# Optimization experiments

Measured on AMD Instinct MI355X. Metric: run time of the kernel, lower is better.

## Reference

```python
import jax, jax.numpy as jnp
import numpy as np

B, S, D_MODEL = 4, 1024, 1024
N_HEAD, D_HEAD = 16, 64
ALL_HEAD = N_HEAD * D_HEAD
SCALE = 1.0 / (D_HEAD ** 0.5)
LN_EPS = 1e-5


def setup_inputs() -> dict:
    key = jax.random.key(0)
    ks = jax.random.split(key, 8)
    inp = jax.random.normal(ks[0], (B, S, D_MODEL), dtype=jnp.float32)
    attn_mask = jax.random.randint(ks[1], (B, S), 0, 2, dtype=jnp.int32)
    w = lambda k, shp: (jax.random.normal(k, shp, dtype=jnp.float32) * 0.02)
    Wq = w(ks[2], (D_MODEL, ALL_HEAD)); bq = jnp.zeros((ALL_HEAD,), jnp.float32)
    Wk = w(ks[3], (D_MODEL, ALL_HEAD)); bk = jnp.zeros((ALL_HEAD,), jnp.float32)
    Wv = w(ks[4], (D_MODEL, ALL_HEAD)); bv = jnp.zeros((ALL_HEAD,), jnp.float32)
    Wo = w(ks[5], (ALL_HEAD, D_MODEL))
    ln_g = jnp.ones((D_MODEL,), jnp.float32)
    ln_b = jnp.zeros((D_MODEL,), jnp.float32)
    return {"inp": inp, "attn_mask": attn_mask, "Wq": Wq, "bq": bq,
            "Wk": Wk, "bk": bk, "Wv": Wv, "bv": bv, "Wo": Wo,
            "ln_g": ln_g, "ln_b": ln_b}


def _layer_norm(x, g, b):
    mu = jnp.mean(x, axis=-1, keepdims=True)
    var = jnp.mean((x - mu) ** 2, axis=-1, keepdims=True)
    return (x - mu) * jax.lax.rsqrt(var + LN_EPS) * g + b


def reference(inp, attn_mask, Wq, bq, Wk, bk, Wv, bv, Wo, ln_g, ln_b):
    residual = inp
    # QKV projections -> [B, S, H, D] -> flat [B*H, S, D] (batch-major, as torch permute+reshape)
    def proj(W, bias):
        h = (inp @ W + bias).reshape(B, S, N_HEAD, D_HEAD)
        return h.transpose(0, 2, 1, 3).reshape(B * N_HEAD, S, D_HEAD)
    q = proj(Wq, bq)
    k = proj(Wk, bk)
    v = proj(Wv, bv)
    # scores [B*H, S, S]
    scores = jnp.einsum('bqd,bkd->bqk', q, k) * SCALE
    # key-padding mask: nonzero -> masked_fill(-100000.0)
    mask = (attn_mask.astype(scores.dtype) != 0)  # [B, S]
    mask = jnp.broadcast_to(mask[:, None, None, :], (B, N_HEAD, S, S))
    mask = mask.reshape(B * N_HEAD, S, S)
    scores = jnp.where(mask, jnp.float32(-100000.0), scores)
    probs = jax.nn.softmax(scores, axis=2)  # dropout is identity in eval
    attn_vec = jnp.einsum('bqk,bkd->bqd', probs, v)  # [B*H, S, D]
    # faithful to torch: view(n_head, B, S, d_head).permute(1,2,0,3)
    attn_vec = attn_vec.reshape(N_HEAD, B, S, D_HEAD).transpose(1, 2, 0, 3)
    attn_vec = attn_vec.reshape(B, S, ALL_HEAD)
    attn_out = attn_vec @ Wo  # o_net has no bias; output dropout identity
    # post-lnorm (pre_lnorm=False)
    return _layer_norm(residual + attn_out, ln_g, ln_b)
```

## Files before the change

### kernel.cpp

```cpp
#include <hip/hip_runtime.h>

typedef __attribute__((ext_vector_type(8))) short bf16x8;
typedef __attribute__((ext_vector_type(4))) float f32x4;
typedef __attribute__((ext_vector_type(16))) float f32x16;

#define D_MODEL 1024
#define SEQ 1024
#define NB 4
#define NH 16
#define DH 64
#define MROWS 4096

__device__ __forceinline__ unsigned short f2bf(float f) {
    union { float f; unsigned u; } x; x.f = f;
    unsigned r = x.u + 0x7fffu + ((x.u >> 16) & 1u);
    return (unsigned short)(r >> 16);
}

__device__ __forceinline__ void gload16(const void* g, void* l) {
    __builtin_amdgcn_global_load_lds((const __attribute__((address_space(1))) void*)g,
                                     (__attribute__((address_space(3))) void*)l, 16, 0, 0);
}

__device__ __forceinline__ float xhalf(float x, int hi) {
    float a = x, b = x;
    asm volatile("v_permlane32_swap_b32 %0, %1" : "+v"(a), "+v"(b));
    return hi ? b : a;
}

__global__ __launch_bounds__(256) void cvt_x(const float* __restrict__ x,
                                             unsigned short* __restrict__ o) {
    int i = blockIdx.x * 256 + threadIdx.x;
    float4 v = ((const float4*)x)[i];
    ushort4 r;
    r.x = f2bf(v.x); r.y = f2bf(v.y); r.z = f2bf(v.z); r.w = f2bf(v.w);
    ((ushort4*)o)[i] = r;
}

__global__ __launch_bounds__(256) void pack_mask(const int* __restrict__ amask,
                                                 unsigned long long* __restrict__ mwords) {
    int word = blockIdx.x * 4 + (threadIdx.x >> 6);
    int lane = threadIdx.x & 63;
    unsigned long long m = __ballot(amask[word * 64 + lane] != 0);
    if (lane == 0) mwords[word] = m;
}

__global__ __launch_bounds__(256) void transpose_w(const float* __restrict__ Wq,
                                                   const float* __restrict__ Wk,
                                                   const float* __restrict__ Wv,
                                                   const float* __restrict__ Wo,
                                                   unsigned short* __restrict__ Wqkv_t,
                                                   unsigned short* __restrict__ Wo_t) {
    __shared__ float tile[32][33];
    const int mtx = blockIdx.z;
    const float* src = mtx == 0 ? Wq : mtx == 1 ? Wk : mtx == 2 ? Wv : Wo;
    unsigned short* dst = mtx < 3 ? (Wqkv_t + (size_t)mtx * D_MODEL * D_MODEL) : Wo_t;
    const int n0 = blockIdx.x * 32, k0 = blockIdx.y * 32;
    const int tx = threadIdx.x, ty = threadIdx.y;
    #pragma unroll
    for (int i = 0; i < 32; i += 8)
        tile[ty + i][tx] = src[(size_t)(k0 + ty + i) * D_MODEL + n0 + tx];
    __syncthreads();
    #pragma unroll
    for (int i = 0; i < 32; i += 8)
        dst[(size_t)(n0 + ty + i) * D_MODEL + k0 + tx] = f2bf(tile[tx][ty + i]);
}

#define CSW(r, c) ((r) * 128 + ((c) ^ (((r) & 7) << 3)))

__global__ __launch_bounds__(256) void gemm_qkv(const unsigned short* __restrict__ Xb,
                                                const unsigned short* __restrict__ Wt,
                                                const float* __restrict__ bq,
                                                const float* __restrict__ bk,
                                                const float* __restrict__ bv,
                                                unsigned short* __restrict__ Qb,
                                                unsigned short* __restrict__ Kb,
                                                unsigned short* __restrict__ Vt) {
    __shared__ unsigned short SM[32768];
    const int tid = threadIdx.x;
    const int lane = tid & 63, wid = tid >> 6;
    const int fr = lane & 15, fg = lane >> 4;
    const int wr = wid >> 1, wc = wid & 1;
    const int lin = blockIdx.x;
    const int x = lin & 7, i = lin >> 3;
    const int bxm = (x & 3) * 8 + (i & 7);
    const int byn = (x >> 2) * 12 + (i >> 3);
    const int m0 = bxm * 128, n0 = byn * 128;
    const unsigned short* Ag = Xb + (size_t)m0 * D_MODEL;
    const unsigned short* Bg = Wt + (size_t)n0 * D_MODEL;
    const int srow = tid >> 3;
    const int scol = 8 * ((tid & 7) ^ ((tid >> 3) & 7));
    f32x4 acc[4][4] = {};

#define QSTAGE(bf, kt2)                                                                   \
    {                                                                                     \
        const int kb = (kt2) * 64;                                                        \
        _Pragma("unroll")                                                                 \
        for (int j = 0; j < 4; ++j) {                                                     \
            int row = j * 32 + srow;                                                      \
            gload16(Ag + (size_t)row * D_MODEL + kb + scol, &SM[(bf) * 16384 + (j * 256 + tid) * 8]); \
            gload16(Bg + (size_t)row * D_MODEL + kb + scol, &SM[(bf) * 16384 + 8192 + (j * 256 + tid) * 8]); \
        }                                                                                 \
    }

    QSTAGE(0, 0);
    __syncthreads();
    int buf = 0;
    for (int kt = 0; kt < 16; ++kt) {
        if (kt < 15) QSTAGE(buf ^ 1, kt + 1);
        const unsigned short* As = &SM[buf * 16384];
        const unsigned short* Bs = &SM[buf * 16384 + 8192];
        #pragma unroll
        for (int ks = 0; ks < 2; ++ks) {
            bf16x8 af[4], bfv[4];
            #pragma unroll
            for (int m = 0; m < 4; ++m) {
                int row = wr * 64 + m * 16 + fr;
                af[m] = *(const bf16x8*)&As[row * 64 + ((ks * 32 + fg * 8) ^ ((row & 7) * 8))];
            }
            #pragma unroll
            for (int n = 0; n < 4; ++n) {
                int row = wc * 64 + n * 16 + fr;
                bfv[n] = *(const bf16x8*)&Bs[row * 64 + ((ks * 32 + fg * 8) ^ ((row & 7) * 8))];
            }
            __builtin_amdgcn_s_setprio(1);
            #pragma unroll
            for (int m = 0; m < 4; ++m)
                #pragma unroll
                for (int n = 0; n < 4; ++n)
                    acc[m][n] = __builtin_amdgcn_mfma_f32_16x16x32_bf16(af[m], bfv[n], acc[m][n], 0, 0, 0);
            __builtin_amdgcn_s_setprio(0);
        }
        __syncthreads();
        buf ^= 1;
    }
#undef QSTAGE
    unsigned short* Cs = SM;
    const int sel = n0 >> 10;
    const int npb = n0 & 1023;
    if (sel < 2) {
        #pragma unroll
        for (int n = 0; n < 4; ++n) {
            int cn = wc * 64 + n * 16 + fr;
            float bias = (sel == 0 ? bq : bk)[npb + cn];
            #pragma unroll
            for (int m = 0; m < 4; ++m)
                #pragma unroll
                for (int r = 0; r < 4; ++r) {
                    int row = wr * 64 + m * 16 + fg * 4 + r;
                    Cs[CSW(row, cn)] = f2bf(acc[m][n][r] + bias);
                }
        }
        __syncthreads();
        unsigned short* dst = sel == 0 ? Qb : Kb;
        #pragma unroll
        for (int k = 0; k < 8; ++k) {
            int c = k * 256 + tid;
            int row = c >> 4, cc = c & 15;
            int np = npb + cc * 8;
            int h = np >> 6, d = np & 63;
            int gm = m0 + row, b = gm >> 10, s = gm & 1023;
            bf16x8 v = *(const bf16x8*)&Cs[CSW(row, cc * 8)];
            *(bf16x8*)&dst[((size_t)(b * NH + h) * SEQ + s) * DH + d] = v;
        }
    } else {
        #pragma unroll
        for (int n = 0; n < 4; ++n) {
            int cn = wc * 64 + n * 16 + fr;
            float bias = bv[npb + cn];
            #pragma unroll
            for (int m = 0; m < 4; ++m)
                #pragma unroll
                for (int r = 0; r < 4; ++r) {
                    int row = wr * 64 + m * 16 + fg * 4 + r;
                    Cs[CSW(cn, row)] = f2bf(acc[m][n][r] + bias);
                }
        }
        __syncthreads();
        #pragma unroll
        for (int k = 0; k < 8; ++k) {
            int c = k * 256 + tid;
            int dcol = c >> 4, scc = c & 15;
            int np = npb + dcol;
            int h = np >> 6, dd = np & 63;
            int gm0 = m0 + scc * 8, b = gm0 >> 10, s0 = gm0 & 1023;
            bf16x8 v = *(const bf16x8*)&Cs[CSW(dcol, scc * 8)];
            *(bf16x8*)&Vt[((size_t)(b * NH + h) * DH + dd) * SEQ + s0] = v;
        }
    }
}

__global__ __launch_bounds__(256) void gemm_o(const unsigned short* __restrict__ Ab,
                                              const unsigned short* __restrict__ Wt,
                                              float* __restrict__ tmp) {
    __shared__ unsigned short SM[32768];
    const int tid = threadIdx.x;
    const int lane = tid & 63, wid = tid >> 6;
    const int fr = lane & 15, fg = lane >> 4;
    const int wr = wid >> 1, wc = wid & 1;
    const int lin = blockIdx.x;
    const int x = lin & 7, i = lin >> 3;
    const int bxm = (x & 3) * 8 + (i & 7);
    const int byn = (x >> 2) * 4 + (i >> 3);
    const int m0 = bxm * 128, n0 = byn * 128;
    const unsigned short* Ag = Ab + (size_t)m0 * D_MODEL;
    const unsigned short* Bg = Wt + (size_t)n0 * D_MODEL;
    const int srow = tid >> 3;
    const int scol = 8 * ((tid & 7) ^ ((tid >> 3) & 7));
    f32x4 acc[4][4] = {};

#define OSTAGE(bf, kt2)                                                                   \
    {                                                                                     \
        const int kb = (kt2) * 64;                                                        \
        _Pragma("unroll")                                                                 \
        for (int j = 0; j < 4; ++j) {                                                     \
            int row = j * 32 + srow;                                                      \
            gload16(Ag + (size_t)row * D_MODEL + kb + scol, &SM[(bf) * 16384 + (j * 256 + tid) * 8]); \
            gload16(Bg + (size_t)row * D_MODEL + kb + scol, &SM[(bf) * 16384 + 8192 + (j * 256 + tid) * 8]); \
        }                                                                                 \
    }

    OSTAGE(0, 0);
    __syncthreads();
    int buf = 0;
    for (int kt = 0; kt < 16; ++kt) {
        if (kt < 15) OSTAGE(buf ^ 1, kt + 1);
        const unsigned short* As = &SM[buf * 16384];
        const unsigned short* Bs = &SM[buf * 16384 + 8192];
        #pragma unroll
        for (int ks = 0; ks < 2; ++ks) {
            bf16x8 af[4], bfv[4];
            #pragma unroll
            for (int m = 0; m < 4; ++m) {
                int row = wr * 64 + m * 16 + fr;
                af[m] = *(const bf16x8*)&As[row * 64 + ((ks * 32 + fg * 8) ^ ((row & 7) * 8))];
            }
            #pragma unroll
            for (int n = 0; n < 4; ++n) {
                int row = wc * 64 + n * 16 + fr;
                bfv[n] = *(const bf16x8*)&Bs[row * 64 + ((ks * 32 + fg * 8) ^ ((row & 7) * 8))];
            }
            __builtin_amdgcn_s_setprio(1);
            #pragma unroll
            for (int m = 0; m < 4; ++m)
                #pragma unroll
                for (int n = 0; n < 4; ++n)
                    acc[m][n] = __builtin_amdgcn_mfma_f32_16x16x32_bf16(af[m], bfv[n], acc[m][n], 0, 0, 0);
            __builtin_amdgcn_s_setprio(0);
        }
        __syncthreads();
        buf ^= 1;
    }
#undef OSTAGE
    #pragma unroll
    for (int n = 0; n < 4; ++n) {
        int gn = n0 + wc * 64 + n * 16 + fr;
        #pragma unroll
        for (int m = 0; m < 4; ++m) {
            #pragma unroll
            for (int r = 0; r < 4; ++r) {
                int gm = m0 + wr * 64 + m * 16 + fg * 4 + r;
                tmp[(size_t)gm * D_MODEL + gn] = acc[m][n][r];
            }
        }
    }
}

__global__ __launch_bounds__(256, 2) void attn_kernel(const unsigned short* __restrict__ Qb,
                                                      const unsigned short* __restrict__ Kb,
                                                      const unsigned short* __restrict__ Vt,
                                                      const unsigned long long* __restrict__ mwords,
                                                      unsigned short* __restrict__ AF) {
    __shared__ unsigned short Ks[2][128 * 64];
    __shared__ unsigned short Vts[2][64 * 128];
    const int tid = threadIdx.x, lane = tid & 63, wid = tid >> 6;
    const int l31 = lane & 31, hi = lane >> 5;
    const int lin = blockIdx.x;
    const int x = lin & 7, i = lin >> 3;
    const int qt = i & 7, bh = x * 8 + (i >> 3);
    const int b = bh >> 4;
    const unsigned short* Qh = Qb + (size_t)bh * SEQ * DH;
    const unsigned short* Kh = Kb + (size_t)bh * SEQ * DH;
    const unsigned short* Vth = Vt + (size_t)bh * DH * SEQ;
    const unsigned long long* mwb = mwords + b * 16;
    const int q0 = qt * 128 + wid * 32;

    const int k_row = wid * 32 + (lane >> 3);
    const int k_col = 8 * ((lane & 7) ^ ((lane >> 3) & 7));
    const int v_rowb = wid * 16 + (lane >> 4);

    bf16x8 qf[4];
    #pragma unroll
    for (int ks = 0; ks < 4; ++ks)
        qf[ks] = *(const bf16x8*)(Qh + (size_t)(q0 + l31) * DH + ks * 16 + hi * 8);

    f32x16 oacc0 = {}, oacc1 = {};
    float mrun = -3.0e38f, lrun = 0.f;
    const float C2 = 0.18033688f;

#define KSWZ(row, colsh) ((row) * 64 + ((colsh) ^ (((row) & 7) << 3)))
#define VSWZ(row, colsh) ((row) * 128 + ((colsh) ^ (((row) & 7) << 3)))
#define STAGE(bufi, kt2)                                                                  \
    {                                                                                     \
        const int kv0s = (kt2) * 128;                                                     \
        _Pragma("unroll")                                                                 \
        for (int j = 0; j < 4; ++j)                                                       \
            gload16(Kh + (size_t)(kv0s + k_row + j * 8) * DH + k_col,                     \
                    &Ks[bufi][wid * 2048 + j * 512]);                                     \
        _Pragma("unroll")                                                                 \
        for (int j = 0; j < 4; ++j) {                                                     \
            const int vr = v_rowb + j * 4;                                                \
            gload16(Vth + (size_t)vr * SEQ + kv0s + 8 * ((lane & 15) ^ (vr & 7)),         \
                    &Vts[bufi][wid * 2048 + j * 512]);                                    \
        }                                                                                 \
    }

    STAGE(0, 0);
    __syncthreads();
    int buf = 0;
    for (int kt = 0; kt < 8; ++kt) {
        if (kt < 7) STAGE(buf ^ 1, kt + 1);
        const unsigned long long mwA = mwb[2 * kt], mwB = mwb[2 * kt + 1];
        const unsigned mflA0 = (unsigned)(mwA >> (4 * hi));
        const unsigned mflA1 = (unsigned)(mwA >> (32 + 4 * hi));
        const unsigned mflB0 = (unsigned)(mwB >> (4 * hi));
        const unsigned mflB1 = (unsigned)(mwB >> (32 + 4 * hi));
        f32x16 sA0 = {}, sA1 = {}, sB0 = {}, sB1 = {};
        __builtin_amdgcn_s_setprio(1);
        #pragma unroll
        for (int ks = 0; ks < 4; ++ks) {
            const int ch = ks * 16 + hi * 8;
            bf16x8 k0 = *(const bf16x8*)&Ks[buf][KSWZ(l31, ch)];
            bf16x8 k1 = *(const bf16x8*)&Ks[buf][KSWZ(32 + l31, ch)];
            bf16x8 k2 = *(const bf16x8*)&Ks[buf][KSWZ(64 + l31, ch)];
            bf16x8 k3 = *(const bf16x8*)&Ks[buf][KSWZ(96 + l31, ch)];
            sA0 = __builtin_amdgcn_mfma_f32_32x32x16_bf16(k0, qf[ks], sA0, 0, 0, 0);
            sA1 = __builtin_amdgcn_mfma_f32_32x32x16_bf16(k1, qf[ks], sA1, 0, 0, 0);
            sB0 = __builtin_amdgcn_mfma_f32_32x32x16_bf16(k2, qf[ks], sB0, 0, 0, 0);
            sB1 = __builtin_amdgcn_mfma_f32_32x32x16_bf16(k3, qf[ks], sB1, 0, 0, 0);
        }
        __builtin_amdgcn_s_setprio(0);
        float tm[16];
        #pragma unroll
        for (int r2 = 0; r2 < 16; ++r2)
            tm[r2] = fmaxf(fmaxf(sA0[r2], sA1[r2]), fmaxf(sB0[r2], sB1[r2]));
        #pragma unroll
        for (int st = 8; st; st >>= 1)
            #pragma unroll
            for (int r2 = 0; r2 < st; ++r2)
                tm[r2] = fmaxf(tm[r2], tm[r2 + st]);
        float m = tm[0];
        m = fmaxf(m, xhalf(m, hi));
        float mt = m * C2;
        if (!__all(mt <= mrun + 11.5f)) {
            float newm = fmaxf(mrun, mt);
            float corr = exp2f(mrun - newm);
            lrun *= corr;
            #pragma unroll
            for (int r2 = 0; r2 < 16; ++r2) { oacc0[r2] *= corr; oacc1[r2] *= corr; }
            mrun = newm;
        }
        float ts[16];
        #pragma unroll
        for (int r2 = 0; r2 < 16; ++r2) {
            const int kvb = (r2 & 3) + 8 * (r2 >> 2);
            float pA0 = exp2f(fmaf(sA0[r2], C2, -mrun));
            float pA1 = exp2f(fmaf(sA1[r2], C2, -mrun));
            float pB0 = exp2f(fmaf(sB0[r2], C2, -mrun));
            float pB1 = exp2f(fmaf(sB1[r2], C2, -mrun));
            pA0 = ((mflA0 >> kvb) & 1) ? 0.f : pA0;
            pA1 = ((mflA1 >> kvb) & 1) ? 0.f : pA1;
            pB0 = ((mflB0 >> kvb) & 1) ? 0.f : pB0;
            pB1 = ((mflB1 >> kvb) & 1) ? 0.f : pB1;
            sA0[r2] = pA0; sA1[r2] = pA1; sB0[r2] = pB0; sB1[r2] = pB1;
            ts[r2] = (pA0 + pA1) + (pB0 + pB1);
        }
        #pragma unroll
        for (int st = 8; st; st >>= 1)
            #pragma unroll
            for (int r2 = 0; r2 < st; ++r2)
                ts[r2] += ts[r2 + st];
        float ps = ts[0];
        ps += xhalf(ps, hi);
        lrun += ps;
        unsigned cA0[8], cA1[8], cB0[8], cB1[8];
        #pragma unroll
        for (int ii = 0; ii < 8; ++ii) {
            asm volatile("v_cvt_pk_bf16_f32 %0, %1, %2" : "=v"(cA0[ii]) : "v"(sA0[2 * ii]), "v"(sA0[2 * ii + 1]));
            asm volatile("v_cvt_pk_bf16_f32 %0, %1, %2" : "=v"(cA1[ii]) : "v"(sA1[2 * ii]), "v"(sA1[2 * ii + 1]));
            asm volatile("v_cvt_pk_bf16_f32 %0, %1, %2" : "=v"(cB0[ii]) : "v"(sB0[2 * ii]), "v"(sB0[2 * ii + 1]));
            asm volatile("v_cvt_pk_bf16_f32 %0, %1, %2" : "=v"(cB1[ii]) : "v"(sB1[2 * ii]), "v"(sB1[2 * ii + 1]));
        }
        #pragma unroll
        for (int g = 0; g < 8; g += 4) {
            asm volatile("v_permlane32_swap_b32 %0, %1" : "+v"(cA0[g + 0]), "+v"(cA0[g + 2]));
            asm volatile("v_permlane32_swap_b32 %0, %1" : "+v"(cA0[g + 1]), "+v"(cA0[g + 3]));
            asm volatile("v_permlane32_swap_b32 %0, %1" : "+v"(cA1[g + 0]), "+v"(cA1[g + 2]));
            asm volatile("v_permlane32_swap_b32 %0, %1" : "+v"(cA1[g + 1]), "+v"(cA1[g + 3]));
            asm volatile("v_permlane32_swap_b32 %0, %1" : "+v"(cB0[g + 0]), "+v"(cB0[g + 2]));
            asm volatile("v_permlane32_swap_b32 %0, %1" : "+v"(cB0[g + 1]), "+v"(cB0[g + 3]));
            asm volatile("v_permlane32_swap_b32 %0, %1" : "+v"(cB1[g + 0]), "+v"(cB1[g + 2]));
            asm volatile("v_permlane32_swap_b32 %0, %1" : "+v"(cB1[g + 1]), "+v"(cB1[g + 3]));
        }
        __builtin_amdgcn_s_setprio(1);
        #pragma unroll
        for (int t = 0; t < 8; ++t) {
            const unsigned* cp = (t < 2) ? cA0 : (t < 4) ? cA1 : (t < 6) ? cB0 : cB1;
            const int g = (t & 1) * 4;
            union { unsigned u[4]; bf16x8 v; } pb;
            pb.u[0] = cp[g + 0]; pb.u[1] = cp[g + 1]; pb.u[2] = cp[g + 2]; pb.u[3] = cp[g + 3];
            const int ch = t * 16 + hi * 8;
            bf16x8 vf0 = *(const bf16x8*)&Vts[buf][VSWZ(l31, ch)];
            bf16x8 vf1 = *(const bf16x8*)&Vts[buf][VSWZ(32 + l31, ch)];
            oacc0 = __builtin_amdgcn_mfma_f32_32x32x16_bf16(vf0, pb.v, oacc0, 0, 0, 0);
            oacc1 = __builtin_amdgcn_mfma_f32_32x32x16_bf16(vf1, pb.v, oacc1, 0, 0, 0);
        }
        __builtin_amdgcn_s_setprio(0);
        __syncthreads();
        buf ^= 1;
    }
#undef STAGE
#undef KSWZ
#undef VSWZ
    const float rl = 1.f / lrun;
    const int b2 = bh & 3, h2 = bh >> 2;
    const size_t rowbase = ((size_t)b2 * SEQ + q0 + l31) * D_MODEL + h2 * 64 + 4 * hi;
    #pragma unroll
    for (int df = 0; df < 2; ++df) {
        const f32x16& oa = df ? oacc1 : oacc0;
        #pragma unroll
        for (int rg = 0; rg < 4; ++rg) {
            ushort4 pk;
            pk.x = f2bf(oa[rg * 4 + 0] * rl);
            pk.y = f2bf(oa[rg * 4 + 1] * rl);
            pk.z = f2bf(oa[rg * 4 + 2] * rl);
            pk.w = f2bf(oa[rg * 4 + 3] * rl);
            *(ushort4*)&AF[rowbase + 32 * df + 8 * rg] = pk;
        }
    }
}

__global__ __launch_bounds__(256) void ln_kernel(const float* __restrict__ tmp,
                                                 const float* __restrict__ inp,
                                                 const float* __restrict__ g,
                                                 const float* __restrict__ bb,
                                                 float* __restrict__ out) {
    __shared__ float red[8];
    const int row = blockIdx.x, tid = threadIdx.x;
    float4 t = ((const float4*)(tmp + (size_t)row * D_MODEL))[tid];
    float4 rr = ((const float4*)(inp + (size_t)row * D_MODEL))[tid];
    float4 y;
    y.x = t.x + rr.x; y.y = t.y + rr.y; y.z = t.z + rr.z; y.w = t.w + rr.w;
    float sum = y.x + y.y + y.z + y.w;
    float sq = y.x * y.x + y.y * y.y + y.z * y.z + y.w * y.w;
    #pragma unroll
    for (int o = 1; o < 64; o <<= 1) { sum += __shfl_xor(sum, o); sq += __shfl_xor(sq, o); }
    int wid = tid >> 6, lane = tid & 63;
    if (lane == 0) { red[wid] = sum; red[4 + wid] = sq; }
    __syncthreads();
    sum = red[0] + red[1] + red[2] + red[3];
    sq = red[4] + red[5] + red[6] + red[7];
    float mu = sum * (1.f / D_MODEL);
    float var = sq * (1.f / D_MODEL) - mu * mu;
    float rs = rsqrtf(var + 1e-5f);
    float4 gg = ((const float4*)g)[tid];
    float4 bv = ((const float4*)bb)[tid];
    float4 o4;
    o4.x = (y.x - mu) * rs * gg.x + bv.x;
    o4.y = (y.y - mu) * rs * gg.y + bv.y;
    o4.z = (y.z - mu) * rs * gg.z + bv.z;
    o4.w = (y.w - mu) * rs * gg.w + bv.w;
    ((float4*)(out + (size_t)row * D_MODEL))[tid] = o4;
}

extern "C" void kernel_launch(void* const* d_in, const int* in_sizes, int n_in,
                              void* d_out, int out_size, void* d_ws, size_t ws_size,
                              hipStream_t stream) {
    const float* inp = (const float*)d_in[0];
    const int* amask = (const int*)d_in[1];
    const float* Wq = (const float*)d_in[2];
    const float* bq = (const float*)d_in[3];
    const float* Wk = (const float*)d_in[4];
    const float* bk = (const float*)d_in[5];
    const float* Wv = (const float*)d_in[6];
    const float* bv = (const float*)d_in[7];
    const float* Wo = (const float*)d_in[8];
    const float* lg = (const float*)d_in[9];
    const float* lb = (const float*)d_in[10];
    float* out = (float*)d_out;
    char* ws = (char*)d_ws;

    unsigned short* Xb     = (unsigned short*)(ws + 0);
    unsigned short* Wqkv_t = (unsigned short*)(ws + 8388608);
    unsigned short* Wo_t   = (unsigned short*)(ws + 14680064);
    unsigned short* Qb     = (unsigned short*)(ws + 16777216);
    unsigned short* Kb     = (unsigned short*)(ws + 25165824);
    unsigned short* Vt     = (unsigned short*)(ws + 33554432);
    unsigned short* AF     = (unsigned short*)(ws + 41943040);
    float*          tmp    = (float*)(ws + 50331648);
    unsigned long long* mwords = (unsigned long long*)(ws + 50331648);

    cvt_x<<<4096, 256, 0, stream>>>(inp, Xb);
    pack_mask<<<16, 256, 0, stream>>>(amask, mwords);
    transpose_w<<<dim3(32, 32, 4), dim3(32, 8), 0, stream>>>(Wq, Wk, Wv, Wo, Wqkv_t, Wo_t);
    gemm_qkv<<<768, 256, 0, stream>>>(Xb, Wqkv_t, bq, bk, bv, Qb, Kb, Vt);
    attn_kernel<<<512, 256, 0, stream>>>(Qb, Kb, Vt, mwords, AF);
    gemm_o<<<256, 256, 0, stream>>>(AF, Wo_t, tmp);
    ln_kernel<<<4096, 256, 0, stream>>>(tmp, inp, lg, lb, out);
}
```

Measured before the change: 115.3 us.

## Offload mask bias and softmax row-sum to MFMA instructions

Masking moves from per-element VALU selects to an extra MFMA per score tile that adds a bf16 large-negative bias to masked key columns. The softmax denominator is no longer a VALU reduction with a cross-lane exchange; it is accumulated by an extra MFMA of a ones matrix against the bf16 probabilities, alongside the PV product. This shifts VALU work onto the matrix unit at the cost of 12 extra MFMAs per tile. It also changes numerics: the masked bias is bf16 (about -100000*scale after scaling), and the row sum now uses bf16-rounded probabilities.

```diff
diff --git a/kernel.cpp b/kernel.cpp
--- a/kernel.cpp
+++ b/kernel.cpp
@@ -294,8 +294,14 @@
     for (int ks = 0; ks < 4; ++ks)
         qf[ks] = *(const bf16x8*)(Qh + (size_t)(q0 + l31) * DH + ks * 16 + hi * 8);
 
+    union U4 { unsigned u[4]; bf16x8 v; };
+    U4 ones;
+    ones.u[0] = 0x3F803F80u; ones.u[1] = 0x3F803F80u;
+    ones.u[2] = 0x3F803F80u; ones.u[3] = 0x3F803F80u;
+
     f32x16 oacc0 = {}, oacc1 = {};
-    float mrun = -3.0e38f, lrun = 0.f;
+    f32x16 sacc = {};
+    float mrun = -3.0e38f;
     const float C2 = 0.18033688f;
 
 #define KSWZ(row, colsh) ((row) * 64 + ((colsh) ^ (((row) & 7) << 3)))
@@ -321,10 +327,8 @@
     for (int kt = 0; kt < 8; ++kt) {
         if (kt < 7) STAGE(buf ^ 1, kt + 1);
         const unsigned long long mwA = mwb[2 * kt], mwB = mwb[2 * kt + 1];
-        const unsigned mflA0 = (unsigned)(mwA >> (4 * hi));
-        const unsigned mflA1 = (unsigned)(mwA >> (32 + 4 * hi));
-        const unsigned mflB0 = (unsigned)(mwB >> (4 * hi));
-        const unsigned mflB1 = (unsigned)(mwB >> (32 + 4 * hi));
+        const unsigned mr0 = (unsigned)mwA, mr1 = (unsigned)(mwA >> 32);
+        const unsigned mr2 = (unsigned)mwB, mr3 = (unsigned)(mwB >> 32);
         f32x16 sA0 = {}, sA1 = {}, sB0 = {}, sB1 = {};
         __builtin_amdgcn_s_setprio(1);
         #pragma unroll
@@ -339,6 +343,18 @@
             sB0 = __builtin_amdgcn_mfma_f32_32x32x16_bf16(k2, qf[ks], sB0, 0, 0, 0);
             sB1 = __builtin_amdgcn_mfma_f32_32x32x16_bf16(k3, qf[ks], sB1, 0, 0, 0);
         }
+        {
+            U4 ab; ab.u[1] = 0; ab.u[2] = 0; ab.u[3] = 0;
+            unsigned bv;
+            bv = ((mr0 >> l31) & 1u) ? 0xC943u : 0u; ab.u[0] = hi ? 0u : bv;
+            sA0 = __builtin_amdgcn_mfma_f32_32x32x16_bf16(ab.v, ones.v, sA0, 0, 0, 0);
+            bv = ((mr1 >> l31) & 1u) ? 0xC943u : 0u; ab.u[0] = hi ? 0u : bv;
+            sA1 = __builtin_amdgcn_mfma_f32_32x32x16_bf16(ab.v, ones.v, sA1, 0, 0, 0);
+            bv = ((mr2 >> l31) & 1u) ? 0xC943u : 0u; ab.u[0] = hi ? 0u : bv;
+            sB0 = __builtin_amdgcn_mfma_f32_32x32x16_bf16(ab.v, ones.v, sB0, 0, 0, 0);
+            bv = ((mr3 >> l31) & 1u) ? 0xC943u : 0u; ab.u[0] = hi ? 0u : bv;
+            sB1 = __builtin_amdgcn_mfma_f32_32x32x16_bf16(ab.v, ones.v, sB1, 0, 0, 0);
+        }
         __builtin_amdgcn_s_setprio(0);
         float tm[16];
         #pragma unroll
@@ -355,34 +371,19 @@
         if (!__all(mt <= mrun + 11.5f)) {
             float newm = fmaxf(mrun, mt);
             float corr = exp2f(mrun - newm);
-            lrun *= corr;
-            #pragma unroll
-            for (int r2 = 0; r2 < 16; ++r2) { oacc0[r2] *= corr; oacc1[r2] *= corr; }
+            #pragma unroll
+            for (int r2 = 0; r2 < 16; ++r2) {
+                oacc0[r2] *= corr; oacc1[r2] *= corr; sacc[r2] *= corr;
+            }
             mrun = newm;
         }
-        float ts[16];
         #pragma unroll
         for (int r2 = 0; r2 < 16; ++r2) {
-            const int kvb = (r2 & 3) + 8 * (r2 >> 2);
-            float pA0 = exp2f(fmaf(sA0[r2], C2, -mrun));
-            float pA1 = exp2f(fmaf(sA1[r2], C2, -mrun));
-            float pB0 = exp2f(fmaf(sB0[r2], C2, -mrun));
-            float pB1 = exp2f(fmaf(sB1[r2], C2, -mrun));
-            pA0 = ((mflA0 >> kvb) & 1) ? 0.f : pA0;
-            pA1 = ((mflA1 >> kvb) & 1) ? 0.f : pA1;
-            pB0 = ((mflB0 >> kvb) & 1) ? 0.f : pB0;
-            pB1 = ((mflB1 >> kvb) & 1) ? 0.f : pB1;
-            sA0[r2] = pA0; sA1[r2] = pA1; sB0[r2] = pB0; sB1[r2] = pB1;
-            ts[r2] = (pA0 + pA1) + (pB0 + pB1);
-        }
-        #pragma unroll
-        for (int st = 8; st; st >>= 1)
-            #pragma unroll
-            for (int r2 = 0; r2 < st; ++r2)
-                ts[r2] += ts[r2 + st];
-        float ps = ts[0];
-        ps += xhalf(ps, hi);
-        lrun += ps;
+            sA0[r2] = exp2f(fmaf(sA0[r2], C2, -mrun));
+            sA1[r2] = exp2f(fmaf(sA1[r2], C2, -mrun));
+            sB0[r2] = exp2f(fmaf(sB0[r2], C2, -mrun));
+            sB1[r2] = exp2f(fmaf(sB1[r2], C2, -mrun));
+        }
         unsigned cA0[8], cA1[8], cB0[8], cB1[8];
         #pragma unroll
         for (int ii = 0; ii < 8; ++ii) {
@@ -407,13 +408,14 @@
         for (int t = 0; t < 8; ++t) {
             const unsigned* cp = (t < 2) ? cA0 : (t < 4) ? cA1 : (t < 6) ? cB0 : cB1;
             const int g = (t & 1) * 4;
-            union { unsigned u[4]; bf16x8 v; } pb;
+            U4 pb;
             pb.u[0] = cp[g + 0]; pb.u[1] = cp[g + 1]; pb.u[2] = cp[g + 2]; pb.u[3] = cp[g + 3];
             const int ch = t * 16 + hi * 8;
             bf16x8 vf0 = *(const bf16x8*)&Vts[buf][VSWZ(l31, ch)];
             bf16x8 vf1 = *(const bf16x8*)&Vts[buf][VSWZ(32 + l31, ch)];
             oacc0 = __builtin_amdgcn_mfma_f32_32x32x16_bf16(vf0, pb.v, oacc0, 0, 0, 0);
             oacc1 = __builtin_amdgcn_mfma_f32_32x32x16_bf16(vf1, pb.v, oacc1, 0, 0, 0);
+            sacc  = __builtin_amdgcn_mfma_f32_32x32x16_bf16(ones.v, pb.v, sacc, 0, 0, 0);
         }
         __builtin_amdgcn_s_setprio(0);
         __syncthreads();
@@ -422,7 +424,7 @@
 #undef STAGE
 #undef KSWZ
 #undef VSWZ
-    const float rl = 1.f / lrun;
+    const float rl = 1.f / sacc[0];
     const int b2 = bh & 3, h2 = bh >> 2;
     const size_t rowbase = ((size_t)b2 * SEQ + q0 + l31) * D_MODEL + h2 * 64 + 4 * hi;
     #pragma unroll
```

After: 108.2 us. 1.07x faster.
